# Optimization experiments

Hardware: AMD Instinct MI355X
Metric: run time of the kernel (lower is better)

The kernel has to match this reference:

```python
import jax, jax.numpy as jnp
import numpy as np

STRIDE = (1, 1)
PAD = (1, 1)

def setup_inputs() -> dict:
    key = jax.random.key(0)
    k1, k2, k3 = jax.random.split(key, 3)
    x = jax.random.normal(k1, (32, 128, 56, 56), dtype=jnp.float32)
    # K ~ N(0,1) per nn.init.normal_(self.K)
    K = jax.random.normal(k2, (256, 128, 3, 3), dtype=jnp.float32)
    bias = jax.random.normal(k3, (1,), dtype=jnp.float32)  # single scalar bias added to whole output
    return {"x": x, "K": K, "bias": bias}

def reference(x, K, bias):
    # Cross-correlation (torch conv semantics), NCHW / OIHW, zero padding.
    y = jax.lax.conv_general_dilated(
        x, K,
        window_strides=STRIDE,
        padding=[(PAD[0], PAD[0]), (PAD[1], PAD[1])],
        dimension_numbers=("NCHW", "OIHW", "NCHW"),
    )
    # Original adds a single scalar bias to the entire output tensor.
    return y + bias
```

## Files before the change

kernel.cpp:

```cpp
#include <hip/hip_runtime.h>

typedef __bf16 bf16x8 __attribute__((ext_vector_type(8)));
typedef float  floatx16 __attribute__((ext_vector_type(16)));

#define HW   56
#define NPIX 3136
#define CIN  128
#define COUT 256

__global__ __launch_bounds__(256) void wt_transform_kernel(
        const float* __restrict__ Kw, __bf16* __restrict__ W2) {
    int idx = blockIdx.x * 256 + threadIdx.x;
    int j     = idx & 7;
    int oc    = (idx >> 3) & 255;
    int cg    = (idx >> 11) & 3;
    int tapcc = idx >> 13;
    int tap   = tapcc % 9;
    int cc    = tapcc / 9;
    int c = cc * 32 + cg * 8 + j;
    W2[idx] = (__bf16)Kw[oc * 1152 + c * 9 + tap];
}

__device__ __forceinline__ int xs_idx(int row, int wp, int cg) {
    return row * 2640 + wp * 40 + cg * 8;
}

__global__ __launch_bounds__(256, 3) void conv_kernel(
        const float* __restrict__ x, const __bf16* __restrict__ W2,
        const float* __restrict__ bias, float* __restrict__ out) {
    __shared__ __align__(16) __bf16 Xs[4 * 2640];

    const int t    = threadIdx.x;
    const int nb   = blockIdx.x / 28;
    const int ht   = blockIdx.x % 28;
    const int h0   = ht * 2;
    const int ocb  = blockIdx.y * 128;

    const int wid  = t >> 6;
    const int lane = t & 63;
    const int half = lane >> 5;
    const int l31  = lane & 31;

    const int oc_base = ocb + (wid & 1) * 64;
    const int prow    = wid >> 1;

    floatx16 acc[2][2];
    #pragma unroll
    for (int mi = 0; mi < 2; ++mi)
        #pragma unroll
        for (int nj = 0; nj < 2; ++nj)
            #pragma unroll
            for (int k = 0; k < 16; ++k)
                acc[mi][nj][k] = 0.f;

    if (t < 160) {
        int cg   = t & 3;
        int rest = t >> 2;
        int row  = rest / 10;
        int zw   = rest % 10;
        int wp   = (zw == 0) ? 0 : (56 + zw);
        *(int4*)&Xs[xs_idx(row, wp, cg)] = make_int4(0, 0, 0, 0);
    }

    const int  sw     = t & 63;
    const int  sg     = t >> 6;
    const bool wvalid = sw < 56;

    for (int cc = 0; cc < 4; ++cc) {
        __syncthreads();
        #pragma unroll
        for (int row = 0; row < 4; ++row) {
            int hin = h0 - 1 + row;
            bf16x8 v;
            #pragma unroll
            for (int j = 0; j < 8; ++j) v[j] = (__bf16)0.f;
            if (wvalid && (unsigned)hin < 56u) {
                const float* src = x + (size_t)(nb * CIN + cc * 32 + sg * 8) * NPIX
                                     + hin * HW + sw;
                #pragma unroll
                for (int j = 0; j < 8; ++j)
                    v[j] = (__bf16)src[j * NPIX];
            }
            if (wvalid)
                *(bf16x8*)&Xs[xs_idx(row, 1 + sw, sg)] = v;
        }
        __syncthreads();

        #pragma unroll
        for (int tap = 0; tap < 9; ++tap) {
            const int r = tap / 3, s = tap % 3;
            const __bf16* wtap = W2 + (size_t)(cc * 9 + tap) * (4 * 256 * 8);
            #pragma unroll
            for (int kc = 0; kc < 2; ++kc) {
                bf16x8 afr[2];
                #pragma unroll
                for (int mi = 0; mi < 2; ++mi) {
                    int oc = oc_base + mi * 32 + l31;
                    afr[mi] = *(const bf16x8*)(wtap + ((kc * 2 + half) * 256 + oc) * 8);
                }
                bf16x8 bfr[2];
                #pragma unroll
                for (int nj = 0; nj < 2; ++nj) {
                    int pw = nj * 32 + l31;
                    bfr[nj] = *(const bf16x8*)&Xs[xs_idx(prow + r, pw + s, kc * 2 + half)];
                }
                #pragma unroll
                for (int mi = 0; mi < 2; ++mi)
                    #pragma unroll
                    for (int nj = 0; nj < 2; ++nj)
                        acc[mi][nj] = __builtin_amdgcn_mfma_f32_32x32x16_bf16(
                            afr[mi], bfr[nj], acc[mi][nj], 0, 0, 0);
            }
        }
    }

    const float bv = bias[0];
    const int hout = h0 + prow;
    #pragma unroll
    for (int nj = 0; nj < 2; ++nj) {
        int pw = nj * 32 + l31;
        if (pw < 56) {
            #pragma unroll
            for (int mi = 0; mi < 2; ++mi) {
                #pragma unroll
                for (int rg = 0; rg < 16; ++rg) {
                    int oc = oc_base + mi * 32 + (rg & 3) + ((rg >> 2) << 3) + half * 4;
                    out[(size_t)(nb * COUT + oc) * NPIX + hout * HW + pw] = acc[mi][nj][rg] + bv;
                }
            }
        }
    }
}

extern "C" void kernel_launch(void* const* d_in, const int* in_sizes, int n_in,
                              void* d_out, int out_size, void* d_ws, size_t ws_size,
                              hipStream_t stream) {
    const float* x    = (const float*)d_in[0];
    const float* Kw   = (const float*)d_in[1];
    const float* bias = (const float*)d_in[2];
    float* out = (float*)d_out;
    __bf16* W2 = (__bf16*)d_ws;

    wt_transform_kernel<<<dim3(1152), dim3(256), 0, stream>>>(Kw, W2);
    conv_kernel<<<dim3(32 * 28, 2), dim3(256), 0, stream>>>(x, W2, bias, out);
}
```

Baseline: 206.9 us.

## Double-buffer input tile in LDS and prefetch next channel chunk into registers

Splits the shared input tile into two buffers. The global loads for the next channel chunk are issued into registers before the current chunk's MFMA loop and written to the other LDS buffer afterwards. This is meant to hide global-load latency behind compute and to remove one barrier per iteration. In exchange it doubles LDS use to about 42KB per block and adds 32 float staging registers, which may lower occupancy below the requested 3 blocks per CU.

```diff
diff --git a/kernel.cpp b/kernel.cpp
--- a/kernel.cpp
+++ b/kernel.cpp
@@ -28,7 +28,7 @@
 __global__ __launch_bounds__(256, 3) void conv_kernel(
         const float* __restrict__ x, const __bf16* __restrict__ W2,
         const float* __restrict__ bias, float* __restrict__ out) {
-    __shared__ __align__(16) __bf16 Xs[4 * 2640];
+    __shared__ __align__(16) __bf16 Xs[2][4 * 2640];
 
     const int t    = threadIdx.x;
     const int nb   = blockIdx.x / 28;
@@ -59,33 +59,51 @@
         int row  = rest / 10;
         int zw   = rest % 10;
         int wp   = (zw == 0) ? 0 : (56 + zw);
-        *(int4*)&Xs[xs_idx(row, wp, cg)] = make_int4(0, 0, 0, 0);
+        *(int4*)&Xs[0][xs_idx(row, wp, cg)] = make_int4(0, 0, 0, 0);
+        *(int4*)&Xs[1][xs_idx(row, wp, cg)] = make_int4(0, 0, 0, 0);
     }
 
     const int  sw     = t & 63;
     const int  sg     = t >> 6;
     const bool wvalid = sw < 56;
 
-    for (int cc = 0; cc < 4; ++cc) {
-        __syncthreads();
+    float stg[4][8];
+
+    auto stage_load = [&](int cc) {
         #pragma unroll
         for (int row = 0; row < 4; ++row) {
             int hin = h0 - 1 + row;
-            bf16x8 v;
             #pragma unroll
-            for (int j = 0; j < 8; ++j) v[j] = (__bf16)0.f;
+            for (int j = 0; j < 8; ++j) stg[row][j] = 0.f;
             if (wvalid && (unsigned)hin < 56u) {
                 const float* src = x + (size_t)(nb * CIN + cc * 32 + sg * 8) * NPIX
                                      + hin * HW + sw;
                 #pragma unroll
                 for (int j = 0; j < 8; ++j)
-                    v[j] = (__bf16)src[j * NPIX];
+                    stg[row][j] = src[j * NPIX];
             }
-            if (wvalid)
-                *(bf16x8*)&Xs[xs_idx(row, 1 + sw, sg)] = v;
         }
-        __syncthreads();
+    };
+    auto stage_write = [&](int buf) {
+        if (wvalid) {
+            #pragma unroll
+            for (int row = 0; row < 4; ++row) {
+                bf16x8 v;
+                #pragma unroll
+                for (int j = 0; j < 8; ++j) v[j] = (__bf16)stg[row][j];
+                *(bf16x8*)&Xs[buf][xs_idx(row, 1 + sw, sg)] = v;
+            }
+        }
+    };
 
+    stage_load(0);
+    stage_write(0);
+    __syncthreads();
+
+    for (int cc = 0; cc < 4; ++cc) {
+        if (cc < 3) stage_load(cc + 1);
+
+        const __bf16* Xb = &Xs[cc & 1][0];
         #pragma unroll
         for (int tap = 0; tap < 9; ++tap) {
             const int r = tap / 3, s = tap % 3;
@@ -102,7 +120,7 @@
                 #pragma unroll
                 for (int nj = 0; nj < 2; ++nj) {
                     int pw = nj * 32 + l31;
-                    bfr[nj] = *(const bf16x8*)&Xs[xs_idx(prow + r, pw + s, kc * 2 + half)];
+                    bfr[nj] = *(const bf16x8*)&Xb[xs_idx(prow + r, pw + s, kc * 2 + half)];
                 }
                 #pragma unroll
                 for (int mi = 0; mi < 2; ++mi)
@@ -111,6 +129,11 @@
                         acc[mi][nj] = __builtin_amdgcn_mfma_f32_32x32x16_bf16(
                             afr[mi], bfr[nj], acc[mi][nj], 0, 0, 0);
             }
+        }
+
+        if (cc < 3) {
+            stage_write((cc + 1) & 1);
+            __syncthreads();
         }
     }
 
```

New measurement: 237.4 us. +14.8%, slower.
